# Kernel tuning notes

Measured on AMD Instinct MI355X. Metric: run time of the kernel, lower is better.

Reference implementation:

```python
import jax, jax.numpy as jnp
import numpy as np

GRID_SIZE = 5
SPLINE_ORDER = 3
HIDDEN = 128
N = 131072
K = 256          # num_cluster
EPS = 1e-8       # torch.cosine_similarity eps
N_COEF = GRID_SIZE + SPLINE_ORDER  # 8 spline basis functions per input feature


def make_grid():
    # efficient-kan grid: grid_range [-1,1], extended by spline_order on each side
    h = 2.0 / GRID_SIZE
    g = jnp.arange(-SPLINE_ORDER, GRID_SIZE + SPLINE_ORDER + 1, dtype=jnp.float32) * h - 1.0
    return jnp.tile(g[None, :], (HIDDEN, 1))  # (in, grid_size + 2*order + 1) = (128, 12)


def b_splines(x, grid):
    # x: (N, in), grid: (in, G) -> bases: (N, in, grid_size + spline_order)
    xe = x[..., None]
    bases = ((xe >= grid[:, :-1]) & (xe < grid[:, 1:])).astype(x.dtype)
    for p in range(1, SPLINE_ORDER + 1):
        left = (xe - grid[:, :-(p + 1)]) / (grid[:, p:-1] - grid[:, :-(p + 1)])
        right = (grid[:, p + 1:] - xe) / (grid[:, p + 1:] - grid[:, 1:-p])
        bases = left * bases[..., :-1] + right * bases[..., 1:]
    return bases


def kan_linear(x, grid, base_w, spline_w, scaler):
    # efficient-kan KANLinear: base path + spline path
    base = jax.nn.silu(x) @ base_w.T                       # (N, out)
    sp = b_splines(x, grid)                                # (N, in, coef)
    sw = spline_w * scaler[..., None]                      # (out, in, coef)
    return base + jnp.einsum('nic,oic->no', sp, sw)


def setup_inputs() -> dict:
    key = jax.random.key(0)
    ks = jax.random.split(key, 9)
    s = 1.0 / np.sqrt(HIDDEN)
    return {
        'x': jax.random.normal(ks[0], (N, HIDDEN), jnp.float32),
        'prototypes': jax.random.normal(ks[1], (K, HIDDEN), jnp.float32),
        'grid': make_grid(),
        'base_w1': jax.random.normal(ks[2], (HIDDEN, HIDDEN), jnp.float32) * s,
        'spline_w1': jax.random.normal(ks[3], (HIDDEN, HIDDEN, N_COEF), jnp.float32) * 0.1,
        'scaler1': jax.random.normal(ks[4], (HIDDEN, HIDDEN), jnp.float32) * s + 1.0,
        'base_w2': jax.random.normal(ks[5], (HIDDEN, HIDDEN), jnp.float32) * s,
        'spline_w2': jax.random.normal(ks[6], (HIDDEN, HIDDEN, N_COEF), jnp.float32) * 0.1,
        'scaler2': jax.random.normal(ks[7], (HIDDEN, HIDDEN), jnp.float32) * s + 1.0,
    }


def reference(x, prototypes, grid, base_w1, spline_w1, scaler1, base_w2, spline_w2, scaler2):
    # KAN([128,128,128]) = two KANLinear layers
    h = kan_linear(x, grid, base_w1, spline_w1, scaler1)
    emb = kan_linear(h, grid, base_w2, spline_w2, scaler2)     # (N, 128)
    # cosine similarity to all prototypes = normalized matmul (same math as
    # the broadcasted torch.cosine_similarity, without the (N,K,H) intermediate)
    xn = emb / jnp.maximum(jnp.linalg.norm(emb, axis=-1, keepdims=True), EPS)
    pn = prototypes / jnp.maximum(jnp.linalg.norm(prototypes, axis=-1, keepdims=True), EPS)
    sim = xn @ pn.T                                            # (N, K)
    cluster_assignments = jnp.argmax(sim, axis=1)              # (N,)
    return emb, cluster_assignments
```

## Files before the change

kernel.cpp:

```cpp
#include <hip/hip_runtime.h>
#include <math.h>

typedef unsigned short u16;
typedef _Float16 f16;
typedef __attribute__((ext_vector_type(8))) _Float16 f16x8;
typedef __attribute__((ext_vector_type(4))) float f32x4;

#define N_ROWS 131072
#define HID 128
#define WS_CH 8192
#define N_WCH 72
#define N_PCH 8

__device__ __forceinline__ void f16_split(float v, f16& hi, f16& lo) {
    f16 h = (f16)v;
    hi = h;
    lo = (f16)(v - (float)h);
}

__device__ __forceinline__ void spline8(float xv, float* a8) {
    float s  = (xv + 2.2f) * 2.5f;
    float tf = floorf(s);
    int   tt = (int)tf;
    bool valid = (tt >= 0) && (tt <= 10);
    float kt = (float)(tt - 3) * 0.4f - 1.0f;
    float u  = (xv - kt) * 2.5f;
    float u2 = u * u, u3 = u2 * u;
    float om = 1.0f - u;
    float b3 = u3 * (1.0f / 6.0f);
    float b2 = (-3.f * u3 + 3.f * u2 + 3.f * u + 1.f) * (1.0f / 6.0f);
    float b1 = (3.f * u3 - 6.f * u2 + 4.f) * (1.0f / 6.0f);
    float b0 = om * om * om * (1.0f / 6.0f);
    #pragma unroll
    for (int c = 0; c < 8; ++c) {
        int d = tt - c;
        float v = 0.f;
        v = (d == 0) ? b3 : v;
        v = (d == 1) ? b2 : v;
        v = (d == 2) ? b1 : v;
        v = (d == 3) ? b0 : v;
        a8[c] = valid ? v : 0.f;
    }
}

#define GLOAD_LDS16(g, l)                                                         \
    __builtin_amdgcn_global_load_lds(                                             \
        (const __attribute__((address_space(1))) unsigned int*)(g),               \
        (__attribute__((address_space(3))) unsigned int*)(l), 16, 0, 0)

__device__ __forceinline__ int tswz(int r, int c) {
    return (r << 7) + ((((c >> 2) ^ r) & 31) << 2) + (c & 3);
}

__global__ __launch_bounds__(256)
void pack_weights(const float* __restrict__ bw1, const float* __restrict__ sw1,
                  const float* __restrict__ sc1,
                  const float* __restrict__ bw2, const float* __restrict__ sw2,
                  const float* __restrict__ sc2,
                  const float* __restrict__ protos, u16* __restrict__ ws)
{
    int gid = blockIdx.x * 256 + threadIdx.x;
    if (gid < N_WCH * 4096) {
        int l  = gid / (36 * 4096);
        int r  = gid % (36 * 4096);
        int ch = r / 4096;
        int e  = r % 4096;
        int o  = e >> 5;
        int kl = e & 31;
        const float* bw = l ? bw2 : bw1;
        const float* sw = l ? sw2 : sw1;
        const float* sc = l ? sc2 : sc1;
        float v;
        if (ch < 4) {
            v = bw[o * HID + ch * 32 + kl];
        } else {
            int i = (ch - 4) * 4 + (kl >> 3);
            v = sw[(o * HID + i) * 8 + (kl & 7)] * sc[o * HID + i];
        }
        f16 hi, lo; f16_split(v, hi, lo);
        int nt = o >> 4, n = o & 15, kq = kl >> 3, c = kl & 7;
        size_t base = (size_t)(l * 36 + ch) * WS_CH;
        size_t idx  = ((size_t)nt * 64 + kq * 16 + n) * 8 + c;
        ws[base + idx]        = __builtin_bit_cast(u16, hi);
        ws[base + 4096 + idx] = __builtin_bit_cast(u16, lo);
    } else if (gid < (N_WCH + N_PCH) * 4096) {
        int r  = gid - N_WCH * 4096;
        int hk = r / 4096;
        int e  = r % 4096;
        int pl = e >> 5;
        int kl = e & 31;
        int half = hk >> 2, kc = hk & 3;
        int p = half * 128 + pl;
        const float4 pv = *(const float4*)(protos + (size_t)p * HID + kl * 4);
        float s = pv.x * pv.x + pv.y * pv.y + pv.z * pv.z + pv.w * pv.w;
        #pragma unroll
        for (int off = 1; off < 32; off <<= 1) s += __shfl_xor(s, off);
        float rp = 1.0f / fmaxf(sqrtf(s), 1e-8f);
        float v = protos[(size_t)p * HID + kc * 32 + kl] * rp;
        f16 hi, lo; f16_split(v, hi, lo);
        int nt = pl >> 4, n = pl & 15, kq = kl >> 3, c = kl & 7;
        size_t base = (size_t)(N_WCH + hk) * WS_CH;
        size_t idx  = ((size_t)nt * 64 + kq * 16 + n) * 8 + c;
        ws[base + idx]        = __builtin_bit_cast(u16, hi);
        ws[base + 4096 + idx] = __builtin_bit_cast(u16, lo);
    }
}

__global__ __launch_bounds__(256, 2)
void kan_fused(const float* __restrict__ x, const u16* __restrict__ wpack,
               float* __restrict__ emb_out, float* __restrict__ assign_out)
{
    __shared__ float t[64 * 128];
    __shared__ u16   Bfrag[2][2][8][64][8];

    const int tid  = threadIdx.x;
    const int lane = tid & 63;
    const int w    = tid >> 6;
    const int m    = lane & 15;
    const int q    = lane >> 4;
    const int row  = w * 16 + m;
    const int brow = blockIdx.x * 64;

#define STAGE(reg_, buf_) do {                                                     \
        const char* _g = (const char*)(wpack + (size_t)(reg_) * WS_CH)             \
                         + w * 4096 + (size_t)lane * 16;                           \
        char* _l = (char*)&Bfrag[(buf_)][0][0][0][0] + w * 4096;                   \
        GLOAD_LDS16(_g,        _l);                                                \
        GLOAD_LDS16(_g + 1024, _l + 1024);                                         \
        GLOAD_LDS16(_g + 2048, _l + 2048);                                         \
        GLOAD_LDS16(_g + 3072, _l + 3072);                                         \
    } while (0)

#define CHUNK_BARRIER() do {                                                       \
        asm volatile("s_waitcnt vmcnt(0)" ::: "memory");                           \
        __builtin_amdgcn_s_barrier();                                              \
        __builtin_amdgcn_sched_barrier(0);                                         \
    } while (0)

    STAGE(0, 0);

    {
        const int m2 = tid >> 2, kq2 = tid & 3;
        const float4* src = (const float4*)(x + (size_t)(brow + m2) * HID + kq2 * 32);
        #pragma unroll
        for (int j = 0; j < 8; ++j) {
            float4 v = src[j];
            *(float4*)&t[tswz(m2, kq2 * 32 + j * 4)] = v;
        }
    }
    CHUNK_BARRIER();

    union { f16x8 v; f16 h[8]; } ah, al, bh, bl;
    f32x4 acc[8];

    for (int l = 0; l < 2; ++l) {
        #pragma unroll
        for (int nt = 0; nt < 8; ++nt) acc[nt] = (f32x4){0.f, 0.f, 0.f, 0.f};

        for (int ch = 0; ch < 36; ++ch) {
            const int reg = l * 36 + ch;
            const int cur = reg & 1;
            STAGE(reg + 1, cur ^ 1);

            float a8[8];
            if (ch < 4) {
                float4 v0 = *(const float4*)&t[tswz(row, ch * 32 + q * 8)];
                float4 v1 = *(const float4*)&t[tswz(row, ch * 32 + q * 8 + 4)];
                float xs[8] = {v0.x, v0.y, v0.z, v0.w, v1.x, v1.y, v1.z, v1.w};
                #pragma unroll
                for (int j = 0; j < 8; ++j)
                    a8[j] = xs[j] * __builtin_amdgcn_rcpf(1.0f + __expf(-xs[j]));
            } else {
                spline8(t[tswz(row, (ch - 4) * 4 + q)], a8);
            }
            #pragma unroll
            for (int j = 0; j < 8; ++j) f16_split(a8[j], ah.h[j], al.h[j]);

            #pragma unroll
            for (int nt = 0; nt < 8; ++nt) {
                bh.v = *(const f16x8*)Bfrag[cur][0][nt][lane];
                bl.v = *(const f16x8*)Bfrag[cur][1][nt][lane];
                acc[nt] = __builtin_amdgcn_mfma_f32_16x16x32_f16(ah.v, bh.v, acc[nt], 0, 0, 0);
                acc[nt] = __builtin_amdgcn_mfma_f32_16x16x32_f16(al.v, bh.v, acc[nt], 0, 0, 0);
                acc[nt] = __builtin_amdgcn_mfma_f32_16x16x32_f16(ah.v, bl.v, acc[nt], 0, 0, 0);
            }
            CHUNK_BARRIER();
        }

        #pragma unroll
        for (int nt = 0; nt < 8; ++nt)
            #pragma unroll
            for (int r = 0; r < 4; ++r)
                t[tswz(w * 16 + q * 4 + r, nt * 16 + m)] = acc[nt][r];
    }

    {
        const int m2 = tid >> 2, kq2 = tid & 3;
        float* dst = emb_out + (size_t)(brow + m2) * HID + kq2 * 32;
        #pragma unroll
        for (int j = 0; j < 8; ++j)
            *(float4*)(dst + j * 4) = *(const float4*)&t[tswz(m2, kq2 * 32 + j * 4)];
    }

    float best[4]; int bi[4];
    #pragma unroll
    for (int r = 0; r < 4; ++r) { best[r] = -3.402823466e+38f; bi[r] = 0; }

    for (int half = 0; half < 2; ++half) {
        #pragma unroll
        for (int nt = 0; nt < 8; ++nt) acc[nt] = (f32x4){0.f, 0.f, 0.f, 0.f};

        for (int kc = 0; kc < 4; ++kc) {
            const int reg = N_WCH + half * 4 + kc;
            const int cur = reg & 1;
            if (reg != 79) STAGE(reg + 1, cur ^ 1);

            float a8[8];
            {
                float4 v0 = *(const float4*)&t[tswz(row, kc * 32 + q * 8)];
                float4 v1 = *(const float4*)&t[tswz(row, kc * 32 + q * 8 + 4)];
                a8[0] = v0.x; a8[1] = v0.y; a8[2] = v0.z; a8[3] = v0.w;
                a8[4] = v1.x; a8[5] = v1.y; a8[6] = v1.z; a8[7] = v1.w;
            }
            #pragma unroll
            for (int j = 0; j < 8; ++j) f16_split(a8[j], ah.h[j], al.h[j]);

            #pragma unroll
            for (int nt = 0; nt < 8; ++nt) {
                bh.v = *(const f16x8*)Bfrag[cur][0][nt][lane];
                bl.v = *(const f16x8*)Bfrag[cur][1][nt][lane];
                acc[nt] = __builtin_amdgcn_mfma_f32_16x16x32_f16(ah.v, bh.v, acc[nt], 0, 0, 0);
                acc[nt] = __builtin_amdgcn_mfma_f32_16x16x32_f16(al.v, bh.v, acc[nt], 0, 0, 0);
                acc[nt] = __builtin_amdgcn_mfma_f32_16x16x32_f16(ah.v, bl.v, acc[nt], 0, 0, 0);
            }
            CHUNK_BARRIER();
        }

        #pragma unroll
        for (int nt = 0; nt < 8; ++nt) {
            int p = half * 128 + nt * 16 + m;
            #pragma unroll
            for (int r = 0; r < 4; ++r) {
                float v = acc[nt][r];
                if (v > best[r]) { best[r] = v; bi[r] = p; }
            }
        }
    }

    #pragma unroll
    for (int r = 0; r < 4; ++r) {
        #pragma unroll
        for (int off = 1; off < 16; off <<= 1) {
            float ov = __shfl_xor(best[r], off);
            int   oi = __shfl_xor(bi[r], off);
            if (ov > best[r] || (ov == best[r] && oi < bi[r])) { best[r] = ov; bi[r] = oi; }
        }
        if (m == 0)
            assign_out[(size_t)brow + w * 16 + q * 4 + r] = (float)bi[r];
    }
#undef STAGE
#undef CHUNK_BARRIER
}

extern "C" void kernel_launch(void* const* d_in, const int* in_sizes, int n_in,
                              void* d_out, int out_size, void* d_ws, size_t ws_size,
                              hipStream_t stream) {
    (void)in_sizes; (void)n_in; (void)out_size; (void)ws_size;

    const float* x      = (const float*)d_in[0];
    const float* protos = (const float*)d_in[1];
    const float* bw1 = (const float*)d_in[3];
    const float* sw1 = (const float*)d_in[4];
    const float* sc1 = (const float*)d_in[5];
    const float* bw2 = (const float*)d_in[6];
    const float* sw2 = (const float*)d_in[7];
    const float* sc2 = (const float*)d_in[8];

    float* out    = (float*)d_out;
    float* embp   = out;
    float* assign = out + (size_t)N_ROWS * HID;
    u16*   wpack  = (u16*)d_ws;

    pack_weights<<<dim3((N_WCH + N_PCH) * 4096 / 256), dim3(256), 0, stream>>>(
        bw1, sw1, sc1, bw2, sw2, sc2, protos, wpack);
    kan_fused<<<dim3(N_ROWS / 64), dim3(256), 0, stream>>>(
        x, wpack, embp, assign);
}
```

Baseline: 434.0 us.

## Stage weight chunks through registers with single LDS buffer and raise occupancy

Replaces the double-buffered global_load_lds weight staging with register prefetch: the next chunk is loaded into VGPRs while the current one is consumed, then written to a single LDS buffer between two barriers. Halving the B-fragment LDS allows launch bounds of 3 blocks per CU. The hi/lo fp16 split now uses packed round-toward-zero conversions, and MFMA sections raise wave priority. Costs are extra registers for the prefetch, two barriers per chunk, and slight rounding differences in the hi split.

Result: faster. 398.2 us (-8.3%).

```diff
diff --git a/kernel.cpp b/kernel.cpp
--- a/kernel.cpp
+++ b/kernel.cpp
@@ -4,6 +4,7 @@
 typedef unsigned short u16;
 typedef _Float16 f16;
 typedef __attribute__((ext_vector_type(8))) _Float16 f16x8;
+typedef __attribute__((ext_vector_type(2))) _Float16 f16x2;
 typedef __attribute__((ext_vector_type(4))) float f32x4;
 
 #define N_ROWS 131072
@@ -12,10 +13,17 @@
 #define N_WCH 72
 #define N_PCH 8
 
-__device__ __forceinline__ void f16_split(float v, f16& hi, f16& lo) {
-    f16 h = (f16)v;
-    hi = h;
-    lo = (f16)(v - (float)h);
+__device__ __forceinline__ void split8(const float* a8, f16x8& hv, f16x8& lv) {
+    union { f16x8 v; f16x2 p[4]; } H, L;
+    #pragma unroll
+    for (int j = 0; j < 4; ++j) {
+        float v0 = a8[2 * j], v1 = a8[2 * j + 1];
+        float h0 = __builtin_bit_cast(float, __builtin_bit_cast(unsigned, v0) & 0xFFFFE000u);
+        float h1 = __builtin_bit_cast(float, __builtin_bit_cast(unsigned, v1) & 0xFFFFE000u);
+        H.p[j] = __builtin_bit_cast(f16x2, __builtin_amdgcn_cvt_pkrtz(v0, v1));
+        L.p[j] = __builtin_bit_cast(f16x2, __builtin_amdgcn_cvt_pkrtz(v0 - h0, v1 - h1));
+    }
+    hv = H.v; lv = L.v;
 }
 
 __device__ __forceinline__ void spline8(float xv, float* a8) {
@@ -42,11 +50,6 @@
         a8[c] = valid ? v : 0.f;
     }
 }
-
-#define GLOAD_LDS16(g, l)                                                         \
-    __builtin_amdgcn_global_load_lds(                                             \
-        (const __attribute__((address_space(1))) unsigned int*)(g),               \
-        (__attribute__((address_space(3))) unsigned int*)(l), 16, 0, 0)
 
 __device__ __forceinline__ int tswz(int r, int c) {
     return (r << 7) + ((((c >> 2) ^ r) & 31) << 2) + (c & 3);
@@ -77,7 +80,8 @@
             int i = (ch - 4) * 4 + (kl >> 3);
             v = sw[(o * HID + i) * 8 + (kl & 7)] * sc[o * HID + i];
         }
-        f16 hi, lo; f16_split(v, hi, lo);
+        f16 hi = (f16)v;
+        f16 lo = (f16)(v - (float)hi);
         int nt = o >> 4, n = o & 15, kq = kl >> 3, c = kl & 7;
         size_t base = (size_t)(l * 36 + ch) * WS_CH;
         size_t idx  = ((size_t)nt * 64 + kq * 16 + n) * 8 + c;
@@ -97,7 +101,8 @@
         for (int off = 1; off < 32; off <<= 1) s += __shfl_xor(s, off);
         float rp = 1.0f / fmaxf(sqrtf(s), 1e-8f);
         float v = protos[(size_t)p * HID + kc * 32 + kl] * rp;
-        f16 hi, lo; f16_split(v, hi, lo);
+        f16 hi = (f16)v;
+        f16 lo = (f16)(v - (float)hi);
         int nt = pl >> 4, n = pl & 15, kq = kl >> 3, c = kl & 7;
         size_t base = (size_t)(N_WCH + hk) * WS_CH;
         size_t idx  = ((size_t)nt * 64 + kq * 16 + n) * 8 + c;
@@ -106,12 +111,12 @@
     }
 }
 
-__global__ __launch_bounds__(256, 2)
+__global__ __launch_bounds__(256, 3)
 void kan_fused(const float* __restrict__ x, const u16* __restrict__ wpack,
                float* __restrict__ emb_out, float* __restrict__ assign_out)
 {
     __shared__ float t[64 * 128];
-    __shared__ u16   Bfrag[2][2][8][64][8];
+    __shared__ u16   Bfrag[2][8][64][8];
 
     const int tid  = threadIdx.x;
     const int lane = tid & 63;
@@ -121,23 +126,29 @@
     const int row  = w * 16 + m;
     const int brow = blockIdx.x * 64;
 
-#define STAGE(reg_, buf_) do {                                                     \
-        const char* _g = (const char*)(wpack + (size_t)(reg_) * WS_CH)             \
-                         + w * 4096 + (size_t)lane * 16;                           \
-        char* _l = (char*)&Bfrag[(buf_)][0][0][0][0] + w * 4096;                   \
-        GLOAD_LDS16(_g,        _l);                                                \
-        GLOAD_LDS16(_g + 1024, _l + 1024);                                         \
-        GLOAD_LDS16(_g + 2048, _l + 2048);                                         \
-        GLOAD_LDS16(_g + 3072, _l + 3072);                                         \
+    const char* gptr = (const char*)wpack + (size_t)w * 4096 + (size_t)lane * 16;
+    uint4* const lptr = (uint4*)&Bfrag[0][0][0][0] + w * 256 + lane;
+    uint4 rr0, rr1, rr2, rr3;
+
+#define ISSUE_LOADS() do {                                                         \
+        rr0 = *(const uint4*)(gptr);                                               \
+        rr1 = *(const uint4*)(gptr + 1024);                                        \
+        rr2 = *(const uint4*)(gptr + 2048);                                        \
+        rr3 = *(const uint4*)(gptr + 3072);                                        \
+        gptr += 16384;                                                             \
     } while (0)
 
-#define CHUNK_BARRIER() do {                                                       \
-        asm volatile("s_waitcnt vmcnt(0)" ::: "memory");                           \
+#define STORE_LDS() do {                                                           \
+        lptr[0] = rr0; lptr[64] = rr1; lptr[128] = rr2; lptr[192] = rr3;           \
+    } while (0)
+
+#define PIPE_BARRIER() do {                                                        \
+        asm volatile("s_waitcnt lgkmcnt(0)" ::: "memory");                         \
         __builtin_amdgcn_s_barrier();                                              \
         __builtin_amdgcn_sched_barrier(0);                                         \
     } while (0)
 
-    STAGE(0, 0);
+    ISSUE_LOADS();
 
     {
         const int m2 = tid >> 2, kq2 = tid & 3;
@@ -148,9 +159,8 @@
             *(float4*)&t[tswz(m2, kq2 * 32 + j * 4)] = v;
         }
     }
-    CHUNK_BARRIER();
-
-    union { f16x8 v; f16 h[8]; } ah, al, bh, bl;
+
+    f16x8 ahv, alv, bhv, blv;
     f32x4 acc[8];
 
     for (int l = 0; l < 2; ++l) {
@@ -158,10 +168,6 @@
         for (int nt = 0; nt < 8; ++nt) acc[nt] = (f32x4){0.f, 0.f, 0.f, 0.f};
 
         for (int ch = 0; ch < 36; ++ch) {
-            const int reg = l * 36 + ch;
-            const int cur = reg & 1;
-            STAGE(reg + 1, cur ^ 1);
-
             float a8[8];
             if (ch < 4) {
                 float4 v0 = *(const float4*)&t[tswz(row, ch * 32 + q * 8)];
@@ -173,18 +179,23 @@
             } else {
                 spline8(t[tswz(row, (ch - 4) * 4 + q)], a8);
             }
-            #pragma unroll
-            for (int j = 0; j < 8; ++j) f16_split(a8[j], ah.h[j], al.h[j]);
-
+            split8(a8, ahv, alv);
+
+            PIPE_BARRIER();
+            STORE_LDS();
+            ISSUE_LOADS();
+            PIPE_BARRIER();
+
+            __builtin_amdgcn_s_setprio(1);
             #pragma unroll
             for (int nt = 0; nt < 8; ++nt) {
-                bh.v = *(const f16x8*)Bfrag[cur][0][nt][lane];
-                bl.v = *(const f16x8*)Bfrag[cur][1][nt][lane];
-                acc[nt] = __builtin_amdgcn_mfma_f32_16x16x32_f16(ah.v, bh.v, acc[nt], 0, 0, 0);
-                acc[nt] = __builtin_amdgcn_mfma_f32_16x16x32_f16(al.v, bh.v, acc[nt], 0, 0, 0);
-                acc[nt] = __builtin_amdgcn_mfma_f32_16x16x32_f16(ah.v, bl.v, acc[nt], 0, 0, 0);
-            }
-            CHUNK_BARRIER();
+                bhv = *(const f16x8*)Bfrag[0][nt][lane];
+                blv = *(const f16x8*)Bfrag[1][nt][lane];
+                acc[nt] = __builtin_amdgcn_mfma_f32_16x16x32_f16(ahv, bhv, acc[nt], 0, 0, 0);
+                acc[nt] = __builtin_amdgcn_mfma_f32_16x16x32_f16(alv, bhv, acc[nt], 0, 0, 0);
+                acc[nt] = __builtin_amdgcn_mfma_f32_16x16x32_f16(ahv, blv, acc[nt], 0, 0, 0);
+            }
+            __builtin_amdgcn_s_setprio(0);
         }
 
         #pragma unroll
@@ -212,8 +223,6 @@
 
         for (int kc = 0; kc < 4; ++kc) {
             const int reg = N_WCH + half * 4 + kc;
-            const int cur = reg & 1;
-            if (reg != 79) STAGE(reg + 1, cur ^ 1);
 
             float a8[8];
             {
@@ -222,18 +231,23 @@
                 a8[0] = v0.x; a8[1] = v0.y; a8[2] = v0.z; a8[3] = v0.w;
                 a8[4] = v1.x; a8[5] = v1.y; a8[6] = v1.z; a8[7] = v1.w;
             }
-            #pragma unroll
-            for (int j = 0; j < 8; ++j) f16_split(a8[j], ah.h[j], al.h[j]);
-
+            split8(a8, ahv, alv);
+
+            PIPE_BARRIER();
+            STORE_LDS();
+            if (reg != 79) ISSUE_LOADS();
+            PIPE_BARRIER();
+
+            __builtin_amdgcn_s_setprio(1);
             #pragma unroll
             for (int nt = 0; nt < 8; ++nt) {
-                bh.v = *(const f16x8*)Bfrag[cur][0][nt][lane];
-                bl.v = *(const f16x8*)Bfrag[cur][1][nt][lane];
-                acc[nt] = __builtin_amdgcn_mfma_f32_16x16x32_f16(ah.v, bh.v, acc[nt], 0, 0, 0);
-                acc[nt] = __builtin_amdgcn_mfma_f32_16x16x32_f16(al.v, bh.v, acc[nt], 0, 0, 0);
-                acc[nt] = __builtin_amdgcn_mfma_f32_16x16x32_f16(ah.v, bl.v, acc[nt], 0, 0, 0);
-            }
-            CHUNK_BARRIER();
+                bhv = *(const f16x8*)Bfrag[0][nt][lane];
+                blv = *(const f16x8*)Bfrag[1][nt][lane];
+                acc[nt] = __builtin_amdgcn_mfma_f32_16x16x32_f16(ahv, bhv, acc[nt], 0, 0, 0);
+                acc[nt] = __builtin_amdgcn_mfma_f32_16x16x32_f16(alv, bhv, acc[nt], 0, 0, 0);
+                acc[nt] = __builtin_amdgcn_mfma_f32_16x16x32_f16(ahv, blv, acc[nt], 0, 0, 0);
+            }
+            __builtin_amdgcn_s_setprio(0);
         }
 
         #pragma unroll
@@ -258,8 +272,9 @@
         if (m == 0)
             assign_out[(size_t)brow + w * 16 + q * 4 + r] = (float)bi[r];
     }
-#undef STAGE
-#undef CHUNK_BARRIER
+#undef ISSUE_LOADS
+#undef STORE_LDS
+#undef PIPE_BARRIER
 }
 
 extern "C" void kernel_launch(void* const* d_in, const int* in_sizes, int n_in,
```
